# Kernel optimization log

Hardware: AMD Instinct MI355X
Metric: run time of the kernel (lower is better)

## Reference

```python
import jax, jax.numpy as jnp
import numpy as np
from jax import lax

ALPHA = 2.0          # HausdorffDistanceLoss alpha
W_CE, W_BD, W_HD = 1.0, 0.5, 0.5   # combined-loss weights
NOSEED = 1e4         # sentinel 1D distance for lines with no seed pixel (>> max real distance)


def _sq_dt_binary(seed):
    """Exact squared 1D distance (along last axis) to nearest True pixel. seed: [..., L] bool."""
    L = seed.shape[-1]
    idx = jnp.arange(L, dtype=jnp.int32)
    left = lax.cummax(jnp.where(seed, idx, -1), axis=seed.ndim - 1)
    right = lax.cummin(jnp.where(seed, idx, 2 * L), axis=seed.ndim - 1, reverse=True)
    dl = jnp.where(left >= 0, (idx - left).astype(jnp.float32), jnp.float32(NOSEED))
    dr = jnp.where(right < 2 * L, (right - idx).astype(jnp.float32), jnp.float32(NOSEED))
    d = jnp.minimum(dl, dr)
    return d * d


def _sq_dt_general(f):
    """d[j] = min_y f[..., y] + (j - y)^2 along last axis (lower envelope, brute force via scan)."""
    L = f.shape[-1]
    idx = jnp.arange(L, dtype=f.dtype)
    fm = jnp.moveaxis(f, -1, 0)  # [L, ...]
    def step(carry, inp):
        fy, y = inp
        cand = fy[..., None] + (idx - y) ** 2  # [..., L]
        return jnp.minimum(carry, cand), None
    init = jnp.full(f.shape, jnp.float32(1e18), f.dtype)
    d, _ = lax.scan(step, init, (fm, idx))
    return d


def edt(seed):
    """Exact 2D Euclidean distance to nearest True pixel. seed: [..., H, W] bool.
    Equivalent to scipy.ndimage.distance_transform_edt(~seed)... i.e. scipy's
    distance_transform_edt(m) == edt(m == 0)."""
    g = jnp.swapaxes(_sq_dt_binary(jnp.swapaxes(seed, -1, -2)), -1, -2)  # pass along H
    return jnp.sqrt(_sq_dt_general(g))  # pass along W


def setup_inputs() -> dict:
    key = jax.random.key(0)
    k1, k2 = jax.random.split(key)
    pred = jax.random.normal(k1, (8, 4, 256, 256), dtype=jnp.float32)
    target = jax.random.randint(k2, (8, 256, 256), 0, 4).astype(jnp.int64)
    return {"pred": pred, "target": target}


def reference(pred, target):
    N, C, H, W = pred.shape
    tgt = target.astype(jnp.int32)

    # --- CrossEntropyLoss (mean over N,H,W) ---
    log_p = jax.nn.log_softmax(pred, axis=1)
    ce = -jnp.mean(jnp.take_along_axis(log_p, tgt[:, None, :, :], axis=1))

    p = jnp.exp(log_p)  # softmax probabilities

    # one-hot target as bool mask [N, C, H, W]
    m = tgt[:, None, :, :] == jnp.arange(C, dtype=jnp.int32)[None, :, None, None]

    # signed distance map: distance_transform_edt(~m) - distance_transform_edt(m)
    dist_to_fg = edt(m)    # == scipy distance_transform_edt(~m): dist to nearest foreground
    dist_to_bg = edt(~m)   # == scipy distance_transform_edt(m):  dist to nearest background
    signed_dm = dist_to_fg - dist_to_bg  # negative inside object

    # --- BoundaryLoss (exclude background channel 0) ---
    bd = jnp.mean(jnp.sum(p[:, 1:] * signed_dm[:, 1:], axis=(2, 3)))

    # --- HausdorffDistanceLoss (exclude background) ---
    dt_gt = dist_to_fg[:, 1:]                     # distance_transform_edt(gt_mask == 0)
    pred_seed = lax.stop_gradient(p[:, 1:]) >= 0.5  # threshold is detached in torch code
    dt_pred = edt(pred_seed)                      # distance_transform_edt(pred < 0.5)
    gt_f = m[:, 1:].astype(p.dtype)
    term1 = jnp.mean(p[:, 1:] * dt_gt ** ALPHA, axis=(2, 3))   # per (n, c) spatial means
    term2 = jnp.mean(gt_f * dt_pred ** ALPHA, axis=(2, 3))
    hd = (jnp.sum(term1) + jnp.sum(term2)) / (2 * N * (C - 1))

    total = W_CE * ce + W_BD * bd + W_HD * hd
    return total, ce, bd, hd
```

## Files before the change

### kernel.cpp

```cpp
#include <hip/hip_runtime.h>

#define NB 8
#define NC 4
#define HH 256
#define WW 256
#define HW_ (HH * WW)
#define NSL 24
#define CT 8
#define NT (WW/CT)

typedef unsigned long long u64;

__device__ inline double block_reduce(double v, double* sbuf) {
  int lane = threadIdx.x & 63;
  int wid  = threadIdx.x >> 6;
  #pragma unroll
  for (int o = 32; o > 0; o >>= 1) v += __shfl_down(v, o, 64);
  if (lane == 0) sbuf[wid] = v;
  __syncthreads();
  double r = 0.0;
  if (threadIdx.x == 0) {
    #pragma unroll
    for (int i = 0; i < 4; ++i) r += sbuf[i];
  }
  __syncthreads();
  return r;
}

__global__ __launch_bounds__(256) void k_softmax_ce(
    const float* __restrict__ pred, const int* __restrict__ tgt,
    float* __restrict__ pbuf, u64* __restrict__ rmT, u64* __restrict__ rmP,
    double* __restrict__ pce) {
  __shared__ double sbuf[4];
  int b = blockIdx.x;
  int n = b >> 8, h = b & (HH - 1);
  int w = threadIdx.x;
  size_t base = (size_t)n * NC * HW_ + (size_t)h * WW + w;
  float x0 = pred[base];
  float x1 = pred[base + HW_];
  float x2 = pred[base + 2 * HW_];
  float x3 = pred[base + 3 * HW_];
  float mx = fmaxf(fmaxf(x0, x1), fmaxf(x2, x3));
  float e0 = expf(x0 - mx), e1 = expf(x1 - mx), e2 = expf(x2 - mx), e3 = expf(x3 - mx);
  float sum = e0 + e1 + e2 + e3;
  float lse = mx + logf(sum);
  int t = tgt[(size_t)n * HW_ + h * WW + w];
  float xt = (t == 0) ? x0 : (t == 1) ? x1 : (t == 2) ? x2 : x3;
  float ce = lse - xt;
  float inv = 1.0f / sum;
  float p1 = e1 * inv, p2 = e2 * inv, p3 = e3 * inv;
  size_t pb = ((size_t)(n * 3)) * HW_ + (size_t)h * WW + w;
  pbuf[pb]           = p1;
  pbuf[pb + HW_]     = p2;
  pbuf[pb + 2 * HW_] = p3;
  u64 bT1 = __ballot(t == 1), bP1 = __ballot(p1 >= 0.5f);
  u64 bT2 = __ballot(t == 2), bP2 = __ballot(p2 >= 0.5f);
  u64 bT3 = __ballot(t == 3), bP3 = __ballot(p3 >= 0.5f);
  if ((threadIdx.x & 63) == 0) {
    int v = threadIdx.x >> 6;
    size_t mi = ((size_t)(n * 3) * HH + h) * 4 + v;
    rmT[mi]                     = bT1;  rmP[mi]                     = bP1;
    rmT[mi + (size_t)HH * 4]     = bT2;  rmP[mi + (size_t)HH * 4]     = bP2;
    rmT[mi + (size_t)2 * HH * 4] = bT3;  rmP[mi + (size_t)2 * HH * 4] = bP3;
  }
  double r = block_reduce((double)ce, sbuf);
  if (threadIdx.x == 0) pce[b] = r;
}

template<int WORD>
__device__ __forceinline__ int nsb(u64 m0, u64 m1, u64 m2, u64 m3, int bit) {
  int dl = 10000, dr = 10000;
  u64 cur = (WORD == 0) ? m0 : (WORD == 1) ? m1 : (WORD == 2) ? m2 : m3;
  u64 below = cur & ((bit == 63) ? ~0ull : ((1ull << (bit + 1)) - 1ull));
  if (below) { dl = bit - (63 - (int)__builtin_clzll(below)); }
  else {
    bool done = false;
    if constexpr (WORD >= 1) {
      u64 x = (WORD == 1) ? m0 : (WORD == 2) ? m1 : m2;
      if (x) { dl = bit + 1 + (int)__builtin_clzll(x); done = true; }
    }
    if constexpr (WORD >= 2) {
      if (!done) { u64 x = (WORD == 2) ? m0 : m1;
        if (x) { dl = bit + 65 + (int)__builtin_clzll(x); done = true; } }
    }
    if constexpr (WORD >= 3) {
      if (!done) { if (m0) dl = bit + 129 + (int)__builtin_clzll(m0); }
    }
    (void)done;
  }
  u64 above = cur & (~0ull << bit);
  if (above) { dr = (int)__builtin_ctzll(above) - bit; }
  else {
    bool done = false;
    if constexpr (WORD <= 2) {
      u64 x = (WORD == 0) ? m1 : (WORD == 1) ? m2 : m3;
      if (x) { dr = 64 + (int)__builtin_ctzll(x) - bit; done = true; }
    }
    if constexpr (WORD <= 1) {
      if (!done) { u64 x = (WORD == 0) ? m2 : m3;
        if (x) { dr = 128 + (int)__builtin_ctzll(x) - bit; done = true; } }
    }
    if constexpr (WORD == 0) {
      if (!done) { if (m3) dr = 192 + (int)__builtin_ctzll(m3) - bit; }
    }
    (void)done;
  }
  return min(dl, dr);
}

template<int WORD>
__device__ __forceinline__ void filltile(
    u64 t0, u64 t1, u64 t2, u64 t3, u64 p0, u64 p1, u64 p2, u64 p3,
    int h, int bit0, float gF[CT][HH], float gB[CT][HH], float gQ[CT][HH],
    unsigned char gtb[CT][HH]) {
  u64 cur = (WORD == 0) ? t0 : (WORD == 1) ? t1 : (WORD == 2) ? t2 : t3;
  #pragma unroll
  for (int wi = 0; wi < CT; ++wi) {
    int bit = bit0 + wi;
    int dF = nsb<WORD>(t0, t1, t2, t3, bit);
    int dB = nsb<WORD>(~t0, ~t1, ~t2, ~t3, bit);
    int dP = nsb<WORD>(p0, p1, p2, p3, bit);
    gF[wi][h] = (float)(dF * dF);
    gB[wi][h] = (float)(dB * dB);
    gQ[wi][h] = (float)(dP * dP);
    gtb[wi][h] = (unsigned char)((cur >> bit) & 1ull);
  }
}

__global__ __launch_bounds__(256) void k_env(
    const u64* __restrict__ rmT, const u64* __restrict__ rmP,
    const float* __restrict__ pbuf, double* __restrict__ part) {
  __shared__ float gF[CT][HH];
  __shared__ float gB[CT][HH];
  __shared__ float gQ[CT][HH];
  __shared__ float pp[CT][HH];
  __shared__ unsigned char gtb[CT][HH];
  __shared__ double sbuf[12];
  int s  = blockIdx.x;
  int w0 = blockIdx.y * CT;
  int h  = threadIdx.x;
  {
    size_t mi = ((size_t)s * HH + h) * 4;
    const ulonglong2* pT = (const ulonglong2*)(rmT + mi);
    const ulonglong2* pP = (const ulonglong2*)(rmP + mi);
    ulonglong2 a0 = pT[0], a1 = pT[1];
    ulonglong2 b0 = pP[0], b1 = pP[1];
    const float* prow = pbuf + (size_t)s * HW_ + (size_t)h * WW + w0;
    float4 pa = *(const float4*)prow;
    float4 pc = *(const float4*)(prow + 4);
    pp[0][h] = pa.x; pp[1][h] = pa.y; pp[2][h] = pa.z; pp[3][h] = pa.w;
    pp[4][h] = pc.x; pp[5][h] = pc.y; pp[6][h] = pc.z; pp[7][h] = pc.w;
    int bit0 = w0 & 63;
    switch (w0 >> 6) {
      case 0: filltile<0>(a0.x,a0.y,a1.x,a1.y,b0.x,b0.y,b1.x,b1.y,h,bit0,gF,gB,gQ,gtb); break;
      case 1: filltile<1>(a0.x,a0.y,a1.x,a1.y,b0.x,b0.y,b1.x,b1.y,h,bit0,gF,gB,gQ,gtb); break;
      case 2: filltile<2>(a0.x,a0.y,a1.x,a1.y,b0.x,b0.y,b1.x,b1.y,h,bit0,gF,gB,gQ,gtb); break;
      default: filltile<3>(a0.x,a0.y,a1.x,a1.y,b0.x,b0.y,b1.x,b1.y,h,bit0,gF,gB,gQ,gtb); break;
    }
  }
  __syncthreads();
  int wi = threadIdx.x & (CT - 1);
  int hg = threadIdx.x / CT;
  double a_bd = 0.0, a_t1 = 0.0, a_t2 = 0.0;
  for (int k = 0; k < 8; ++k) {
    int h2 = hg * 8 + k;
    float mF = gF[wi][h2], mB = gB[wi][h2], mQ = gQ[wi][h2];
    for (int r = 1; r < HH; ++r) {
      float rr = (float)(r * r);
      if (rr >= mF) break;
      int u = h2 - r, d = h2 + r;
      if (u >= 0) mF = fminf(mF, gF[wi][u] + rr);
      if (d < HH) mF = fminf(mF, gF[wi][d] + rr);
    }
    for (int r = 1; r < HH; ++r) {
      float rr = (float)(r * r);
      if (rr >= mB) break;
      int u = h2 - r, d = h2 + r;
      if (u >= 0) mB = fminf(mB, gB[wi][u] + rr);
      if (d < HH) mB = fminf(mB, gB[wi][d] + rr);
    }
    for (int r = 1; r < HH; ++r) {
      float rr = (float)(r * r);
      if (rr >= mQ) break;
      int u = h2 - r, d = h2 + r;
      if (u >= 0) mQ = fminf(mQ, gQ[wi][u] + rr);
      if (d < HH) mQ = fminf(mQ, gQ[wi][d] + rr);
    }
    float dfg = sqrtf(mF), dbg = sqrtf(mB), dpr = sqrtf(mQ);
    float p  = pp[wi][h2];
    float gt = (float)gtb[wi][h2];
    a_bd += (double)(p * (dfg - dbg));
    a_t1 += (double)(p * dfg * dfg);
    a_t2 += (double)(gt * dpr * dpr);
  }
  int lane = threadIdx.x & 63, wid = threadIdx.x >> 6;
  #pragma unroll
  for (int o = 32; o > 0; o >>= 1) {
    a_bd += __shfl_down(a_bd, o, 64);
    a_t1 += __shfl_down(a_t1, o, 64);
    a_t2 += __shfl_down(a_t2, o, 64);
  }
  if (lane == 0) { sbuf[wid*3] = a_bd; sbuf[wid*3+1] = a_t1; sbuf[wid*3+2] = a_t2; }
  __syncthreads();
  if (threadIdx.x == 0) {
    double b = 0, t1 = 0, t2 = 0;
    #pragma unroll
    for (int i = 0; i < 4; ++i) { b += sbuf[i*3]; t1 += sbuf[i*3+1]; t2 += sbuf[i*3+2]; }
    size_t pi = ((size_t)s * NT + blockIdx.y) * 4;
    part[pi] = b; part[pi+1] = t1; part[pi+2] = t2;
  }
}

__global__ __launch_bounds__(256) void k_final(const double* __restrict__ pce,
    const double* __restrict__ part, float* __restrict__ out) {
  __shared__ double sb[16];
  int t = threadIdx.x;
  double ce = 0.0, bd = 0.0, t1 = 0.0, t2 = 0.0;
  for (int i = t; i < NB * HH; i += 256) ce += pce[i];
  for (int i = t; i < NSL * NT; i += 256) {
    bd += part[(size_t)i * 4];
    t1 += part[(size_t)i * 4 + 1];
    t2 += part[(size_t)i * 4 + 2];
  }
  int lane = t & 63, wid = t >> 6;
  #pragma unroll
  for (int o = 32; o > 0; o >>= 1) {
    ce += __shfl_down(ce, o, 64);
    bd += __shfl_down(bd, o, 64);
    t1 += __shfl_down(t1, o, 64);
    t2 += __shfl_down(t2, o, 64);
  }
  if (lane == 0) { sb[wid*4]=ce; sb[wid*4+1]=bd; sb[wid*4+2]=t1; sb[wid*4+3]=t2; }
  __syncthreads();
  if (t == 0) {
    double c = 0, b = 0, u1 = 0, u2 = 0;
    #pragma unroll
    for (int i = 0; i < 4; ++i) { c += sb[i*4]; b += sb[i*4+1]; u1 += sb[i*4+2]; u2 += sb[i*4+3]; }
    c /= (double)(NB * HW_);
    b /= (double)NSL;
    double hd = (u1 + u2) / ((double)HW_ * (double)(2 * NB * (NC - 1)));
    out[0] = (float)(c + 0.5 * b + 0.5 * hd);
    out[1] = (float)c;
    out[2] = (float)b;
    out[3] = (float)hd;
  }
}

extern "C" void kernel_launch(void* const* d_in, const int* in_sizes, int n_in,
                              void* d_out, int out_size, void* d_ws, size_t ws_size,
                              hipStream_t stream) {
  (void)in_sizes; (void)n_in; (void)out_size; (void)ws_size;
  const float* pred = (const float*)d_in[0];
  const int*   tgt  = (const int*)d_in[1];
  float* out = (float*)d_out;
  char* ws = (char*)d_ws;
  double* pce  = (double*)ws;
  double* part = (double*)(ws + 16384);
  float*  pbuf = (float*)(ws + 65536);
  u64* rmT = (u64*)(ws + 65536 + (size_t)NSL * HW_ * 4);
  u64* rmP = rmT + (size_t)NSL * HH * 4;

  hipLaunchKernelGGL(k_softmax_ce, dim3(NB * HH), dim3(256), 0, stream,
                     pred, tgt, pbuf, rmT, rmP, pce);
  hipLaunchKernelGGL(k_env, dim3(NSL, NT), dim3(256), 0, stream,
                     rmT, rmP, pbuf, part);
  hipLaunchKernelGGL(k_final, dim3(1), dim3(256), 0, stream, pce, part, out);
}
```

Before: 90.58 us.

## Incremental row distances, padded shared arrays, per-wave CE partials, fast math

The tile fill now computes left and right 1D seed distances once per tile with bit scans and propagates them incrementally across the 8 columns, instead of doing a full nearest-set-bit search for every column. Shared arrays get padded rows to reduce LDS bank conflicts. The softmax kernel drops its block-level reduction and its two __syncthreads, writing one CE partial per wave, so the final kernel sums four times more partials. Fast __expf and __logf intrinsics replace expf and logf, which risks small precision differences.

```diff
diff --git a/kernel.cpp b/kernel.cpp
--- a/kernel.cpp
+++ b/kernel.cpp
@@ -8,30 +8,14 @@
 #define NSL 24
 #define CT 8
 #define NT (WW/CT)
+#define HP (HH + 1)
 
 typedef unsigned long long u64;
-
-__device__ inline double block_reduce(double v, double* sbuf) {
-  int lane = threadIdx.x & 63;
-  int wid  = threadIdx.x >> 6;
-  #pragma unroll
-  for (int o = 32; o > 0; o >>= 1) v += __shfl_down(v, o, 64);
-  if (lane == 0) sbuf[wid] = v;
-  __syncthreads();
-  double r = 0.0;
-  if (threadIdx.x == 0) {
-    #pragma unroll
-    for (int i = 0; i < 4; ++i) r += sbuf[i];
-  }
-  __syncthreads();
-  return r;
-}
 
 __global__ __launch_bounds__(256) void k_softmax_ce(
     const float* __restrict__ pred, const int* __restrict__ tgt,
     float* __restrict__ pbuf, u64* __restrict__ rmT, u64* __restrict__ rmP,
     double* __restrict__ pce) {
-  __shared__ double sbuf[4];
   int b = blockIdx.x;
   int n = b >> 8, h = b & (HH - 1);
   int w = threadIdx.x;
@@ -41,9 +25,10 @@
   float x2 = pred[base + 2 * HW_];
   float x3 = pred[base + 3 * HW_];
   float mx = fmaxf(fmaxf(x0, x1), fmaxf(x2, x3));
-  float e0 = expf(x0 - mx), e1 = expf(x1 - mx), e2 = expf(x2 - mx), e3 = expf(x3 - mx);
+  float e0 = __expf(x0 - mx), e1 = __expf(x1 - mx);
+  float e2 = __expf(x2 - mx), e3 = __expf(x3 - mx);
   float sum = e0 + e1 + e2 + e3;
-  float lse = mx + logf(sum);
+  float lse = mx + __logf(sum);
   int t = tgt[(size_t)n * HW_ + h * WW + w];
   float xt = (t == 0) ? x0 : (t == 1) ? x1 : (t == 2) ? x2 : x3;
   float ce = lse - xt;
@@ -56,85 +41,110 @@
   u64 bT1 = __ballot(t == 1), bP1 = __ballot(p1 >= 0.5f);
   u64 bT2 = __ballot(t == 2), bP2 = __ballot(p2 >= 0.5f);
   u64 bT3 = __ballot(t == 3), bP3 = __ballot(p3 >= 0.5f);
+  int v = threadIdx.x >> 6;
   if ((threadIdx.x & 63) == 0) {
-    int v = threadIdx.x >> 6;
     size_t mi = ((size_t)(n * 3) * HH + h) * 4 + v;
-    rmT[mi]                     = bT1;  rmP[mi]                     = bP1;
+    rmT[mi]                      = bT1;  rmP[mi]                      = bP1;
     rmT[mi + (size_t)HH * 4]     = bT2;  rmP[mi + (size_t)HH * 4]     = bP2;
     rmT[mi + (size_t)2 * HH * 4] = bT3;  rmP[mi + (size_t)2 * HH * 4] = bP3;
   }
-  double r = block_reduce((double)ce, sbuf);
-  if (threadIdx.x == 0) pce[b] = r;
+  double cd = (double)ce;
+  #pragma unroll
+  for (int o = 32; o > 0; o >>= 1) cd += __shfl_down(cd, o, 64);
+  if ((threadIdx.x & 63) == 0) pce[(b << 2) | v] = cd;
 }
 
 template<int WORD>
-__device__ __forceinline__ int nsb(u64 m0, u64 m1, u64 m2, u64 m3, int bit) {
-  int dl = 10000, dr = 10000;
+__device__ __forceinline__ int nsb_left(u64 m0, u64 m1, u64 m2, u64 m3, int bit) {
   u64 cur = (WORD == 0) ? m0 : (WORD == 1) ? m1 : (WORD == 2) ? m2 : m3;
   u64 below = cur & ((bit == 63) ? ~0ull : ((1ull << (bit + 1)) - 1ull));
-  if (below) { dl = bit - (63 - (int)__builtin_clzll(below)); }
-  else {
-    bool done = false;
-    if constexpr (WORD >= 1) {
-      u64 x = (WORD == 1) ? m0 : (WORD == 2) ? m1 : m2;
-      if (x) { dl = bit + 1 + (int)__builtin_clzll(x); done = true; }
-    }
-    if constexpr (WORD >= 2) {
-      if (!done) { u64 x = (WORD == 2) ? m0 : m1;
-        if (x) { dl = bit + 65 + (int)__builtin_clzll(x); done = true; } }
-    }
-    if constexpr (WORD >= 3) {
-      if (!done) { if (m0) dl = bit + 129 + (int)__builtin_clzll(m0); }
-    }
-    (void)done;
-  }
+  if (below) return bit - (63 - (int)__builtin_clzll(below));
+  if constexpr (WORD >= 1) {
+    u64 x = (WORD == 1) ? m0 : (WORD == 2) ? m1 : m2;
+    if (x) return bit + 1 + (int)__builtin_clzll(x);
+  }
+  if constexpr (WORD >= 2) {
+    u64 x = (WORD == 2) ? m0 : m1;
+    if (x) return bit + 65 + (int)__builtin_clzll(x);
+  }
+  if constexpr (WORD >= 3) {
+    if (m0) return bit + 129 + (int)__builtin_clzll(m0);
+  }
+  return 10000;
+}
+
+template<int WORD>
+__device__ __forceinline__ int nsb_right(u64 m0, u64 m1, u64 m2, u64 m3, int bit) {
+  u64 cur = (WORD == 0) ? m0 : (WORD == 1) ? m1 : (WORD == 2) ? m2 : m3;
   u64 above = cur & (~0ull << bit);
-  if (above) { dr = (int)__builtin_ctzll(above) - bit; }
-  else {
-    bool done = false;
-    if constexpr (WORD <= 2) {
-      u64 x = (WORD == 0) ? m1 : (WORD == 1) ? m2 : m3;
-      if (x) { dr = 64 + (int)__builtin_ctzll(x) - bit; done = true; }
-    }
-    if constexpr (WORD <= 1) {
-      if (!done) { u64 x = (WORD == 0) ? m2 : m3;
-        if (x) { dr = 128 + (int)__builtin_ctzll(x) - bit; done = true; } }
-    }
-    if constexpr (WORD == 0) {
-      if (!done) { if (m3) dr = 192 + (int)__builtin_ctzll(m3) - bit; }
-    }
-    (void)done;
-  }
-  return min(dl, dr);
+  if (above) return (int)__builtin_ctzll(above) - bit;
+  if constexpr (WORD <= 2) {
+    u64 x = (WORD == 0) ? m1 : (WORD == 1) ? m2 : m3;
+    if (x) return 64 + (int)__builtin_ctzll(x) - bit;
+  }
+  if constexpr (WORD <= 1) {
+    u64 x = (WORD == 0) ? m2 : m3;
+    if (x) return 128 + (int)__builtin_ctzll(x) - bit;
+  }
+  if constexpr (WORD == 0) {
+    if (m3) return 192 + (int)__builtin_ctzll(m3) - bit;
+  }
+  return 10000;
 }
 
 template<int WORD>
 __device__ __forceinline__ void filltile(
     u64 t0, u64 t1, u64 t2, u64 t3, u64 p0, u64 p1, u64 p2, u64 p3,
-    int h, int bit0, float gF[CT][HH], float gB[CT][HH], float gQ[CT][HH],
-    unsigned char gtb[CT][HH]) {
-  u64 cur = (WORD == 0) ? t0 : (WORD == 1) ? t1 : (WORD == 2) ? t2 : t3;
+    int h, int bit0, float gF[CT][HP], float gB[CT][HP], float gQ[CT][HP],
+    unsigned char gtb[CT][HH + 4]) {
+  u64 b0 = ~t0, b1 = ~t1, b2 = ~t2, b3 = ~t3;
+  u64 curT = (WORD == 0) ? t0 : (WORD == 1) ? t1 : (WORD == 2) ? t2 : t3;
+  u64 curP = (WORD == 0) ? p0 : (WORD == 1) ? p1 : (WORD == 2) ? p2 : p3;
+  int dF[CT], dB[CT], dQ[CT];
+  int lF = nsb_left<WORD>(t0, t1, t2, t3, bit0);
+  int lB = nsb_left<WORD>(b0, b1, b2, b3, bit0);
+  int lP = nsb_left<WORD>(p0, p1, p2, p3, bit0);
   #pragma unroll
   for (int wi = 0; wi < CT; ++wi) {
     int bit = bit0 + wi;
-    int dF = nsb<WORD>(t0, t1, t2, t3, bit);
-    int dB = nsb<WORD>(~t0, ~t1, ~t2, ~t3, bit);
-    int dP = nsb<WORD>(p0, p1, p2, p3, bit);
-    gF[wi][h] = (float)(dF * dF);
-    gB[wi][h] = (float)(dB * dB);
-    gQ[wi][h] = (float)(dP * dP);
-    gtb[wi][h] = (unsigned char)((cur >> bit) & 1ull);
+    int sF = (int)((curT >> bit) & 1ull);
+    int sP = (int)((curP >> bit) & 1ull);
+    if (wi > 0) {
+      lF = sF ? 0 : min(lF + 1, 10000);
+      lB = sF ? min(lB + 1, 10000) : 0;
+      lP = sP ? 0 : min(lP + 1, 10000);
+    }
+    dF[wi] = lF; dB[wi] = lB; dQ[wi] = lP;
+  }
+  int rF = nsb_right<WORD>(t0, t1, t2, t3, bit0 + CT - 1);
+  int rB = nsb_right<WORD>(b0, b1, b2, b3, bit0 + CT - 1);
+  int rP = nsb_right<WORD>(p0, p1, p2, p3, bit0 + CT - 1);
+  #pragma unroll
+  for (int wi = CT - 1; wi >= 0; --wi) {
+    int bit = bit0 + wi;
+    int sF = (int)((curT >> bit) & 1ull);
+    int sP = (int)((curP >> bit) & 1ull);
+    if (wi < CT - 1) {
+      rF = sF ? 0 : min(rF + 1, 10000);
+      rB = sF ? min(rB + 1, 10000) : 0;
+      rP = sP ? 0 : min(rP + 1, 10000);
+    }
+    int vF = min(dF[wi], rF), vB = min(dB[wi], rB), vQ = min(dQ[wi], rP);
+    gF[wi][h] = (float)(vF * vF);
+    gB[wi][h] = (float)(vB * vB);
+    gQ[wi][h] = (float)(vQ * vQ);
+    gtb[wi][h] = (unsigned char)sF;
   }
 }
 
 __global__ __launch_bounds__(256) void k_env(
     const u64* __restrict__ rmT, const u64* __restrict__ rmP,
     const float* __restrict__ pbuf, double* __restrict__ part) {
-  __shared__ float gF[CT][HH];
-  __shared__ float gB[CT][HH];
-  __shared__ float gQ[CT][HH];
-  __shared__ float pp[CT][HH];
-  __shared__ unsigned char gtb[CT][HH];
+  __shared__ float gF[CT][HP];
+  __shared__ float gB[CT][HP];
+  __shared__ float gQ[CT][HP];
+  __shared__ float pp[CT][HP];
+  __shared__ unsigned char gtb[CT][HH + 4];
   __shared__ double sbuf[12];
   int s  = blockIdx.x;
   int w0 = blockIdx.y * CT;
@@ -144,7 +154,7 @@
     const ulonglong2* pT = (const ulonglong2*)(rmT + mi);
     const ulonglong2* pP = (const ulonglong2*)(rmP + mi);
     ulonglong2 a0 = pT[0], a1 = pT[1];
-    ulonglong2 b0 = pP[0], b1 = pP[1];
+    ulonglong2 c0 = pP[0], c1 = pP[1];
     const float* prow = pbuf + (size_t)s * HW_ + (size_t)h * WW + w0;
     float4 pa = *(const float4*)prow;
     float4 pc = *(const float4*)(prow + 4);
@@ -152,15 +162,15 @@
     pp[4][h] = pc.x; pp[5][h] = pc.y; pp[6][h] = pc.z; pp[7][h] = pc.w;
     int bit0 = w0 & 63;
     switch (w0 >> 6) {
-      case 0: filltile<0>(a0.x,a0.y,a1.x,a1.y,b0.x,b0.y,b1.x,b1.y,h,bit0,gF,gB,gQ,gtb); break;
-      case 1: filltile<1>(a0.x,a0.y,a1.x,a1.y,b0.x,b0.y,b1.x,b1.y,h,bit0,gF,gB,gQ,gtb); break;
-      case 2: filltile<2>(a0.x,a0.y,a1.x,a1.y,b0.x,b0.y,b1.x,b1.y,h,bit0,gF,gB,gQ,gtb); break;
-      default: filltile<3>(a0.x,a0.y,a1.x,a1.y,b0.x,b0.y,b1.x,b1.y,h,bit0,gF,gB,gQ,gtb); break;
+      case 0: filltile<0>(a0.x,a0.y,a1.x,a1.y,c0.x,c0.y,c1.x,c1.y,h,bit0,gF,gB,gQ,gtb); break;
+      case 1: filltile<1>(a0.x,a0.y,a1.x,a1.y,c0.x,c0.y,c1.x,c1.y,h,bit0,gF,gB,gQ,gtb); break;
+      case 2: filltile<2>(a0.x,a0.y,a1.x,a1.y,c0.x,c0.y,c1.x,c1.y,h,bit0,gF,gB,gQ,gtb); break;
+      default: filltile<3>(a0.x,a0.y,a1.x,a1.y,c0.x,c0.y,c1.x,c1.y,h,bit0,gF,gB,gQ,gtb); break;
     }
   }
   __syncthreads();
   int wi = threadIdx.x & (CT - 1);
-  int hg = threadIdx.x / CT;
+  int hg = threadIdx.x >> 3;
   double a_bd = 0.0, a_t1 = 0.0, a_t2 = 0.0;
   for (int k = 0; k < 8; ++k) {
     int h2 = hg * 8 + k;
@@ -216,7 +226,7 @@
   __shared__ double sb[16];
   int t = threadIdx.x;
   double ce = 0.0, bd = 0.0, t1 = 0.0, t2 = 0.0;
-  for (int i = t; i < NB * HH; i += 256) ce += pce[i];
+  for (int i = t; i < NB * HH * 4; i += 256) ce += pce[i];
   for (int i = t; i < NSL * NT; i += 256) {
     bd += part[(size_t)i * 4];
     t1 += part[(size_t)i * 4 + 1];
@@ -255,9 +265,9 @@
   float* out = (float*)d_out;
   char* ws = (char*)d_ws;
   double* pce  = (double*)ws;
-  double* part = (double*)(ws + 16384);
-  float*  pbuf = (float*)(ws + 65536);
-  u64* rmT = (u64*)(ws + 65536 + (size_t)NSL * HW_ * 4);
+  double* part = (double*)(ws + 65536);
+  float*  pbuf = (float*)(ws + 131072);
+  u64* rmT = (u64*)(ws + 131072 + (size_t)NSL * HW_ * 4);
   u64* rmP = rmT + (size_t)NSL * HH * 4;
 
   hipLaunchKernelGGL(k_softmax_ce, dim3(NB * HH), dim3(256), 0, stream,
```

Result: no change. 91.74 us (+1.3%).
